# Performance work log

Measured on AMD Instinct MI355X. Metric: run time of the kernel, lower is better.

## Reference

```python
import jax, jax.numpy as jnp
import numpy as np

S, B, I, H, L, D = 512, 64, 128, 256, 6, 2  # seq, batch, input, hidden, layers, directions


def setup_inputs() -> dict:
    key = jax.random.key(0)
    ks = jax.random.split(key, 7)
    stdv = 1.0 / np.sqrt(H)
    u = lambda k, shape: jax.random.uniform(k, shape, jnp.float32, -stdv, stdv)
    return {
        "x": jax.random.normal(ks[0], (S, B, I), jnp.float32),
        "h0": jax.random.normal(ks[1], (L * D, B, H), jnp.float32),
        "w_ih0": u(ks[2], (D, 3 * H, I)),            # layer 0 input weights
        "w_ih": u(ks[3], (L - 1, D, 3 * H, D * H)),  # layers 1.. input weights
        "w_hh": u(ks[4], (L, D, 3 * H, H)),
        "b_ih": u(ks[5], (L, D, 3 * H)),
        "b_hh": u(ks[6], (L, D, 3 * H)),
    }


def _gru_direction(gate_x, w_hh, b_hh, h0, reverse):
    # gate_x: (S, B, 3H) precomputed x @ W_ih.T + b_ih; scan the recurrence.
    def step(h, gx):
        gh = h @ w_hh.T + b_hh  # (B, 3H)
        x_r, x_z, x_n = jnp.split(gx, 3, axis=-1)
        h_r, h_z, h_n = jnp.split(gh, 3, axis=-1)
        r = jax.nn.sigmoid(x_r + h_r)
        z = jax.nn.sigmoid(x_z + h_z)
        n = jnp.tanh(x_n + r * h_n)
        h_new = (1.0 - z) * n + z * h
        return h_new, h_new

    h_last, ys = jax.lax.scan(step, h0, gate_x, reverse=reverse)
    return h_last, ys  # ys aligned with input time order even when reverse=True


def reference(x, h0, w_ih0, w_ih, w_hh, b_ih, b_hh):
    num_layers = w_hh.shape[0]
    inp = x  # (S, B, in_dim)
    h_n = []
    for layer in range(num_layers):
        outs = []
        for d in range(2):
            w = w_ih0[d] if layer == 0 else w_ih[layer - 1, d]
            # Single GEMM over the whole sequence for the input gates.
            gate_x = jnp.einsum('sbi,gi->sbg', inp, w) + b_ih[layer, d]
            h_last, ys = _gru_direction(
                gate_x, w_hh[layer, d], b_hh[layer, d],
                h0[layer * 2 + d], reverse=(d == 1))
            outs.append(ys)
            h_n.append(h_last)
        inp = jnp.concatenate(outs, axis=-1)  # (S, B, 2H)
    return jnp.stack(h_n)  # (L*2, B, H)
```

## Files before the change

kernel.cpp:

```cpp
#include <hip/hip_runtime.h>
#include <stdint.h>

#define S_LEN 512
#define NB    64
#define HID   256
#define G3    768
#define SB    32768
#define NLAYER 6

typedef short bf16x8 __attribute__((ext_vector_type(8)));
typedef short bf16x4 __attribute__((ext_vector_type(4)));
typedef float floatx4 __attribute__((ext_vector_type(4)));
typedef unsigned short u16;
typedef unsigned int   u32;

__device__ __forceinline__ float bf2f(u16 v) {
  u32 u = ((u32)v) << 16;
  return __builtin_bit_cast(float, u);
}
__device__ __forceinline__ u16 f2bf(float f) {
  u32 u = __builtin_bit_cast(u32, f);
  u = (u + 0x7FFFu + ((u >> 16) & 1u)) >> 16;
  return (u16)u;
}
__device__ __forceinline__ float fsigmoid(float x) {
  return __builtin_amdgcn_rcpf(1.0f + __expf(-x));
}
__device__ __forceinline__ float ftanh(float x) {
  return 1.0f - 2.0f * __builtin_amdgcn_rcpf(1.0f + __expf(x + x));
}
__device__ __forceinline__ u32 pk_bf16(float lo, float hi) {
  u32 r;
  asm("v_cvt_pk_bf16_f32 %0, %1, %2" : "=v"(r) : "v"(lo), "v"(hi));
  return r;
}

__device__ __forceinline__ void lds_barrier() {
  asm volatile("s_waitcnt lgkmcnt(0)\n\ts_barrier" ::: "memory");
}

__global__ void detect_fp32(const u16* __restrict__ x, int n, int* flag) {
  __shared__ int tot;
  if (threadIdx.x == 0) tot = 0;
  __syncthreads();
  int c = 0;
  for (int i = threadIdx.x; i < n; i += blockDim.x) {
    u16 v = x[i];
    if (((v >> 7) & 0xFF) == 0xFF) ++c;
  }
  atomicAdd(&tot, c);
  __syncthreads();
  if (threadIdx.x == 0) *flag = (tot > 64) ? 1 : 0;
}

__global__ void cvt(const void* __restrict__ src, u16* __restrict__ dst,
                    int n, const int* __restrict__ flag) {
  const int stride = gridDim.x * blockDim.x;
  const bool isf32 = (*flag != 0);
  for (int i = blockIdx.x * blockDim.x + threadIdx.x; i < n; i += stride) {
    if (isf32) dst[i] = f2bf(((const float*)src)[i]);
    else       dst[i] = ((const u16*)src)[i];
  }
}

__global__ void prep_bias(const u16* __restrict__ bih, const u16* __restrict__ bhh,
                          float* __restrict__ bc, int n) {
  int i = blockIdx.x * blockDim.x + threadIdx.x;
  if (i >= n) return;
  int col = i % G3;
  float v = bf2f(bih[i]);
  if (col < 512) v += bf2f(bhh[i]);
  bc[i] = v;
}

__global__ void write_out(const float* __restrict__ hNs, void* __restrict__ out,
                          int n, const int* __restrict__ flag) {
  int i = blockIdx.x * blockDim.x + threadIdx.x;
  if (i >= n) return;
  if (*flag) ((float*)out)[i] = hNs[i];
  else       ((u16*)out)[i]   = f2bf(hNs[i]);
}

__global__ __launch_bounds__(256)
void gate_gemm(const u16* __restrict__ A, const u16* __restrict__ W,
               const float* __restrict__ bias, u16* __restrict__ outg, int K) {
  const int m0  = blockIdx.x * 128;
  const int n0  = blockIdx.y * 128;
  const int dir = blockIdx.z;
  W    += (size_t)dir * G3 * K;
  bias += (size_t)dir * G3;
  outg += (size_t)dir * (size_t)SB * G3;

  __shared__ __align__(16) u16 lA[8192];
  __shared__ __align__(16) u16 lB[8192];

  const int tid  = threadIdx.x;
  const int lane = tid & 63;
  const int wv   = tid >> 6;
  const int wm   = wv & 1, wn = wv >> 1;
  const int l15  = lane & 15, quad = lane >> 4;

  floatx4 acc[4][4] = {};

  for (int k0 = 0; k0 < K; k0 += 64) {
    bf16x8 ra[4], rb[4];
#pragma unroll
    for (int i = 0; i < 4; ++i) {
      int c   = i * 256 + tid;
      int row = c >> 3;
      int kc  = (c & 7) ^ (row & 7);
      ra[i] = *(const bf16x8*)(A + (size_t)(m0 + row) * K + (k0 + kc * 8));
      rb[i] = *(const bf16x8*)(W + (size_t)(n0 + row) * K + (k0 + kc * 8));
    }
    __syncthreads();
#pragma unroll
    for (int i = 0; i < 4; ++i) {
      *(bf16x8*)(lA + (size_t)(i * 256 + tid) * 8) = ra[i];
      *(bf16x8*)(lB + (size_t)(i * 256 + tid) * 8) = rb[i];
    }
    __syncthreads();

#pragma unroll
    for (int kt = 0; kt < 2; ++kt) {
      bf16x8 af[4], bfr[4];
#pragma unroll
      for (int mt = 0; mt < 4; ++mt) {
        int row = wm * 64 + mt * 16 + l15;
        int ch  = row * 8 + ((kt * 4 + quad) ^ (row & 7));
        af[mt] = *(const bf16x8*)(lA + ch * 8);
      }
#pragma unroll
      for (int nt = 0; nt < 4; ++nt) {
        int row = wn * 64 + nt * 16 + l15;
        int ch  = row * 8 + ((kt * 4 + quad) ^ (row & 7));
        bfr[nt] = *(const bf16x8*)(lB + ch * 8);
      }
#pragma unroll
      for (int mt = 0; mt < 4; ++mt)
#pragma unroll
        for (int nt = 0; nt < 4; ++nt)
          acc[mt][nt] = __builtin_amdgcn_mfma_f32_16x16x32_bf16(
              af[mt], bfr[nt], acc[mt][nt], 0, 0, 0);
    }
  }

  const int sIdx = (m0 >> 6) + wm;
#pragma unroll
  for (int nt = 0; nt < 4; ++nt) {
    int n    = n0 + wn * 64 + nt * 16 + l15;
    int g    = n >> 8, jc = n & 255;
    float bv = bias[n];
#pragma unroll
    for (int mt = 0; mt < 4; ++mt) {
      bf16x4 pk;
#pragma unroll
      for (int r = 0; r < 4; ++r) pk[r] = (short)f2bf(acc[mt][nt][r] + bv);
      *(bf16x4*)(outg + ((((size_t)mt * 512 + sIdx) * 256 + jc) * 3 + g) * 16 +
                 quad * 4) = pk;
    }
  }
}

__global__ __launch_bounds__(512)
__attribute__((amdgpu_waves_per_eu(2, 2)))
void gru_scan(const u16* __restrict__ gateX,
              const u16* __restrict__ Whh,
              const u16* __restrict__ Bhh,
              const u16* __restrict__ H0,
              u16* __restrict__ layerOut,
              float* __restrict__ hNs,
              int layer) {
  const int dir = blockIdx.x & 1;
  const int bg  = blockIdx.x >> 1;
  const int tid = threadIdx.x;
  const int lane = tid & 63;
  const int wv   = tid >> 6;
  const int l15  = lane & 15, quad = lane >> 4;

  __shared__ __align__(16) u16 wnL[65536];
  __shared__ __align__(16) u16 hb2[2][4096];

  const u16* Wd = Whh + (size_t)dir * G3 * HID;

#pragma unroll
  for (int i = 0; i < 16; ++i) {
    int ci = i * 512 + tid;
    int n  = ci >> 5;
    int c  = ci & 31;
    bf16x8 v = *(const bf16x8*)(Wd + (size_t)(512 + n) * HID + c * 8);
    *(bf16x8*)(wnL + c * 2048 + n * 8) = v;
  }

  bf16x8 wrz[8][2][2];
#pragma unroll
  for (int g = 0; g < 2; ++g)
#pragma unroll
    for (int nt = 0; nt < 2; ++nt) {
      int n = g * 256 + wv * 32 + nt * 16 + l15;
#pragma unroll
      for (int kt = 0; kt < 8; ++kt)
        wrz[kt][g][nt] = *(const bf16x8*)(Wd + (size_t)n * HID + kt * 32 + quad * 8);
    }
#pragma unroll
  for (int kt = 0; kt < 8; ++kt)
#pragma unroll
    for (int g = 0; g < 2; ++g)
#pragma unroll
      for (int nt = 0; nt < 2; ++nt)
        asm volatile("" : "+v"(wrz[kt][g][nt]));

  float bhn[2];
#pragma unroll
  for (int nt = 0; nt < 2; ++nt)
    bhn[nt] = bf2f(Bhh[dir * G3 + 512 + wv * 32 + nt * 16 + l15]);

  const int mrow = quad * 4;
  const int b0   = bg * 16 + mrow;

  const int afb    = quad * 128 + l15 * 8;
  const int bnb0   = quad * 2048 + (wv * 32 + l15) * 8;
  const int bnb1   = bnb0 + 16 * 8;
  int wb[2];
#pragma unroll
  for (int nt = 0; nt < 2; ++nt)
    wb[nt] = (wv * 4 + nt * 2 + (l15 >> 3)) * 128 + quad * 32 + (l15 & 7);

  {
    int row = tid >> 5, slot = tid & 31;
    const u16* hp = H0 + ((size_t)(layer * 2 + dir) * NB + bg * 16 + row) * HID + slot * 8;
    *(bf16x8*)(&hb2[0][slot * 128 + row * 8]) = *(const bf16x8*)hp;
  }
  float hreg[2][4];
#pragma unroll
  for (int nt = 0; nt < 2; ++nt)
#pragma unroll
    for (int r = 0; r < 4; ++r)
      hreg[nt][r] = bf2f(H0[((size_t)(layer * 2 + dir) * NB + b0 + r) * HID +
                            wv * 32 + nt * 16 + l15]);

  const long sstep = dir ? -(long)(256 * 3 * 16) : (long)(256 * 3 * 16);
  const u16* xb;
  {
    const int s0 = dir ? (S_LEN - 1) : 0;
    xb = gateX + (size_t)dir * SB * G3 +
         ((((size_t)bg * 512 + s0) * 256 + (wv * 32 + l15)) * 3) * 16 + quad * 4;
  }
  bf16x4 xp[3][2];
#pragma unroll
  for (int g = 0; g < 3; ++g)
#pragma unroll
    for (int nt = 0; nt < 2; ++nt)
      xp[g][nt] = *(const bf16x4*)(xb + nt * 768 + g * 16);
  xb += sstep;

  u16* loPtr;
  {
    int row = tid >> 5, slot = tid & 31;
    const int sFirst = dir ? (S_LEN - 1) : 0;
    loPtr = layerOut + ((size_t)sFirst * NB + bg * 16 + row) * 512 +
            dir * HID + slot * 8;
  }
  const long lostep = dir ? -(long)(NB * 512) : (long)(NB * 512);

  lds_barrier();

  for (int t = 0; t < S_LEN; ++t) {
    const int cur = t & 1, nxt = cur ^ 1;

    floatx4 aR[2], aZ[2], aN[2];
    bf16x4 xn0 = xp[2][0], xn1 = xp[2][1];
#pragma unroll
    for (int nt = 0; nt < 2; ++nt)
#pragma unroll
      for (int r = 0; r < 4; ++r) {
        aR[nt][r] = bf2f((u16)xp[0][nt][r]);
        aZ[nt][r] = bf2f((u16)xp[1][nt][r]);
        aN[nt][r] = bhn[nt];
      }

#pragma unroll
    for (int g = 0; g < 3; ++g)
#pragma unroll
      for (int nt = 0; nt < 2; ++nt)
        xp[g][nt] = *(const bf16x4*)(xb + nt * 768 + g * 16);
    if (t < S_LEN - 1) xb += sstep;

    if (t > 0) {
      int row = tid >> 5, slot = tid & 31;
      bf16x8 hv = *(const bf16x8*)(&hb2[cur][slot * 128 + row * 8]);
      *(bf16x8*)loPtr = hv;
      loPtr += lostep;
    }

#pragma unroll
    for (int kt = 0; kt < 8; ++kt) {
      bf16x8 af  = *(const bf16x8*)(&hb2[cur][afb + kt * 512]);
      bf16x8 bn0 = *(const bf16x8*)(wnL + bnb0 + kt * 8192);
      bf16x8 bn1 = *(const bf16x8*)(wnL + bnb1 + kt * 8192);
      aR[0] = __builtin_amdgcn_mfma_f32_16x16x32_bf16(af, wrz[kt][0][0], aR[0], 0, 0, 0);
      aR[1] = __builtin_amdgcn_mfma_f32_16x16x32_bf16(af, wrz[kt][0][1], aR[1], 0, 0, 0);
      aZ[0] = __builtin_amdgcn_mfma_f32_16x16x32_bf16(af, wrz[kt][1][0], aZ[0], 0, 0, 0);
      aZ[1] = __builtin_amdgcn_mfma_f32_16x16x32_bf16(af, wrz[kt][1][1], aZ[1], 0, 0, 0);
      aN[0] = __builtin_amdgcn_mfma_f32_16x16x32_bf16(af, bn0,           aN[0], 0, 0, 0);
      aN[1] = __builtin_amdgcn_mfma_f32_16x16x32_bf16(af, bn1,           aN[1], 0, 0, 0);
    }

#pragma unroll
    for (int nt = 0; nt < 2; ++nt) {
      const bf16x4 xn = nt ? xn1 : xn0;
#pragma unroll
      for (int r = 0; r < 4; ++r) {
        float rg = fsigmoid(aR[nt][r]);
        float zg = fsigmoid(aZ[nt][r]);
        float ng = ftanh(bf2f((u16)xn[r]) + rg * aN[nt][r]);
        float hn = ng + zg * (hreg[nt][r] - ng);
        hreg[nt][r] = hn;
        hb2[nxt][wb[nt] + r * 8] = f2bf(hn);
      }
    }

    lds_barrier();
  }

  {
    int row = tid >> 5, slot = tid & 31;
    const int sLast = dir ? 0 : (S_LEN - 1);
    bf16x8 hv = *(const bf16x8*)(&hb2[0][slot * 128 + row * 8]);
    *(bf16x8*)(layerOut + ((size_t)sLast * NB + bg * 16 + row) * 512 +
               dir * HID + slot * 8) = hv;
  }
#pragma unroll
  for (int nt = 0; nt < 2; ++nt)
#pragma unroll
    for (int r = 0; r < 4; ++r)
      hNs[((size_t)(layer * 2 + dir) * NB + b0 + r) * HID +
          wv * 32 + nt * 16 + l15] = hreg[nt][r];
}

extern "C" void kernel_launch(void* const* d_in, const int* in_sizes, int n_in,
                              void* d_out, int out_size, void* d_ws, size_t ws_size,
                              hipStream_t stream) {
  (void)n_in; (void)ws_size;
  char* ws = (char*)d_ws;
  int*   flag  = (int*)ws;
  float* hNs   = (float*)(ws + 4096);
  float* biasC = (float*)(ws + 790528);
  u16*   h0C   = (u16*)(ws + (1u << 20));
  u16*   wih0C = h0C   + 196608;
  u16*   wihC  = wih0C + 196608;
  u16*   whhC  = wihC  + 3932160;
  u16*   bihC  = whhC  + 2359296;
  u16*   bhhC  = bihC  + 9216;
  u16*   gateX = (u16*)(ws + (16u  << 20));
  u16*   bufA  = (u16*)(ws + (112u << 20));
  u16*   bufB  = (u16*)(ws + (144u << 20));
  u16*   xC    = bufB;

  detect_fp32<<<1, 1024, 0, stream>>>((const u16*)d_in[0], 262144, flag);
  cvt<<<512, 256, 0, stream>>>(d_in[0], xC,    in_sizes[0], flag);
  cvt<<<256, 256, 0, stream>>>(d_in[1], h0C,   in_sizes[1], flag);
  cvt<<<256, 256, 0, stream>>>(d_in[2], wih0C, in_sizes[2], flag);
  cvt<<<512, 256, 0, stream>>>(d_in[3], wihC,  in_sizes[3], flag);
  cvt<<<512, 256, 0, stream>>>(d_in[4], whhC,  in_sizes[4], flag);
  cvt<<< 64, 256, 0, stream>>>(d_in[5], bihC,  in_sizes[5], flag);
  cvt<<< 64, 256, 0, stream>>>(d_in[6], bhhC,  in_sizes[6], flag);
  prep_bias<<<36, 256, 0, stream>>>(bihC, bhhC, biasC, NLAYER * 2 * G3);

  for (int layer = 0; layer < NLAYER; ++layer) {
    const u16* inp = (layer == 0) ? xC : ((layer & 1) ? bufA : bufB);
    u16* outBuf    = (layer & 1) ? bufB : bufA;

    const int K = (layer == 0) ? 128 : 512;
    const u16* W = (layer == 0) ? wih0C
                                : (wihC + (size_t)(layer - 1) * 2 * G3 * 512);
    dim3 grid(256, 6, 2);
    gate_gemm<<<grid, 256, 0, stream>>>(inp, W, biasC + (size_t)layer * 2 * G3,
                                        gateX, K);
    gru_scan<<<8, 512, 0, stream>>>(gateX, whhC + (size_t)layer * 2 * G3 * HID,
                                    bhhC + (size_t)layer * 2 * G3, h0C,
                                    outBuf, hNs, layer);
  }
  write_out<<<(out_size + 255) / 256, 256, 0, stream>>>(hNs, d_out, out_size, flag);
}
```

Baseline: 5.964 ms.

## Keep most of W_hn in registers and drop fp32 hidden-state registers

The n-gate recurrent weights for the first six of eight K-tiles now live in VGPRs, and only the last two K-tiles stay in LDS. This shrinks the LDS footprint and cuts per-step LDS traffic in the MFMA loop. To free registers, the fp32 hidden state is no longer carried across steps; it is re-read from the bf16 LDS buffer each step, and the final h_n is written from bf16. The trade is higher register pressure and reduced precision of the carried state, since the blend now uses a bf16-rounded previous h.

```diff
diff --git a/kernel.cpp b/kernel.cpp
--- a/kernel.cpp
+++ b/kernel.cpp
@@ -28,11 +28,6 @@
 }
 __device__ __forceinline__ float ftanh(float x) {
   return 1.0f - 2.0f * __builtin_amdgcn_rcpf(1.0f + __expf(x + x));
-}
-__device__ __forceinline__ u32 pk_bf16(float lo, float hi) {
-  u32 r;
-  asm("v_cvt_pk_bf16_f32 %0, %1, %2" : "=v"(r) : "v"(lo), "v"(hi));
-  return r;
 }
 
 __device__ __forceinline__ void lds_barrier() {
@@ -177,21 +172,22 @@
   const int wv   = tid >> 6;
   const int l15  = lane & 15, quad = lane >> 4;
 
-  __shared__ __align__(16) u16 wnL[65536];
+  __shared__ __align__(16) u16 wnL[16384];
   __shared__ __align__(16) u16 hb2[2][4096];
 
   const u16* Wd = Whh + (size_t)dir * G3 * HID;
 
 #pragma unroll
-  for (int i = 0; i < 16; ++i) {
+  for (int i = 0; i < 4; ++i) {
     int ci = i * 512 + tid;
-    int n  = ci >> 5;
-    int c  = ci & 31;
-    bf16x8 v = *(const bf16x8*)(Wd + (size_t)(512 + n) * HID + c * 8);
-    *(bf16x8*)(wnL + c * 2048 + n * 8) = v;
+    int n  = ci >> 3;
+    int kc = ci & 7;
+    bf16x8 v = *(const bf16x8*)(Wd + (size_t)(512 + n) * HID + (24 + kc) * 8);
+    *(bf16x8*)(wnL + kc * 2048 + n * 8) = v;
   }
 
   bf16x8 wrz[8][2][2];
+  bf16x8 wn6[6][2];
 #pragma unroll
   for (int g = 0; g < 2; ++g)
 #pragma unroll
@@ -202,24 +198,32 @@
         wrz[kt][g][nt] = *(const bf16x8*)(Wd + (size_t)n * HID + kt * 32 + quad * 8);
     }
 #pragma unroll
+  for (int nt = 0; nt < 2; ++nt) {
+    int n = 512 + wv * 32 + nt * 16 + l15;
+#pragma unroll
+    for (int kt = 0; kt < 6; ++kt)
+      wn6[kt][nt] = *(const bf16x8*)(Wd + (size_t)n * HID + kt * 32 + quad * 8);
+  }
+#pragma unroll
   for (int kt = 0; kt < 8; ++kt)
 #pragma unroll
     for (int g = 0; g < 2; ++g)
 #pragma unroll
       for (int nt = 0; nt < 2; ++nt)
         asm volatile("" : "+v"(wrz[kt][g][nt]));
+#pragma unroll
+  for (int kt = 0; kt < 6; ++kt)
+#pragma unroll
+    for (int nt = 0; nt < 2; ++nt)
+      asm volatile("" : "+v"(wn6[kt][nt]));
 
   float bhn[2];
 #pragma unroll
   for (int nt = 0; nt < 2; ++nt)
     bhn[nt] = bf2f(Bhh[dir * G3 + 512 + wv * 32 + nt * 16 + l15]);
 
-  const int mrow = quad * 4;
-  const int b0   = bg * 16 + mrow;
-
-  const int afb    = quad * 128 + l15 * 8;
-  const int bnb0   = quad * 2048 + (wv * 32 + l15) * 8;
-  const int bnb1   = bnb0 + 16 * 8;
+  const int afb = quad * 128 + l15 * 8;
+  const int bnb = quad * 2048 + (wv * 32 + l15) * 8;
   int wb[2];
 #pragma unroll
   for (int nt = 0; nt < 2; ++nt)
@@ -230,13 +234,6 @@
     const u16* hp = H0 + ((size_t)(layer * 2 + dir) * NB + bg * 16 + row) * HID + slot * 8;
     *(bf16x8*)(&hb2[0][slot * 128 + row * 8]) = *(const bf16x8*)hp;
   }
-  float hreg[2][4];
-#pragma unroll
-  for (int nt = 0; nt < 2; ++nt)
-#pragma unroll
-    for (int r = 0; r < 4; ++r)
-      hreg[nt][r] = bf2f(H0[((size_t)(layer * 2 + dir) * NB + b0 + r) * HID +
-                            wv * 32 + nt * 16 + l15]);
 
   const long sstep = dir ? -(long)(256 * 3 * 16) : (long)(256 * 3 * 16);
   const u16* xb;
@@ -285,6 +282,13 @@
         xp[g][nt] = *(const bf16x4*)(xb + nt * 768 + g * 16);
     if (t < S_LEN - 1) xb += sstep;
 
+    u16 hp[2][4];
+#pragma unroll
+    for (int nt = 0; nt < 2; ++nt)
+#pragma unroll
+      for (int r = 0; r < 4; ++r)
+        hp[nt][r] = hb2[cur][wb[nt] + r * 8];
+
     if (t > 0) {
       int row = tid >> 5, slot = tid & 31;
       bf16x8 hv = *(const bf16x8*)(&hb2[cur][slot * 128 + row * 8]);
@@ -294,9 +298,15 @@
 
 #pragma unroll
     for (int kt = 0; kt < 8; ++kt) {
-      bf16x8 af  = *(const bf16x8*)(&hb2[cur][afb + kt * 512]);
-      bf16x8 bn0 = *(const bf16x8*)(wnL + bnb0 + kt * 8192);
-      bf16x8 bn1 = *(const bf16x8*)(wnL + bnb1 + kt * 8192);
+      bf16x8 af = *(const bf16x8*)(&hb2[cur][afb + kt * 512]);
+      bf16x8 bn0, bn1;
+      if (kt < 6) {
+        bn0 = wn6[kt][0];
+        bn1 = wn6[kt][1];
+      } else {
+        bn0 = *(const bf16x8*)(wnL + bnb + (kt - 6) * 8192);
+        bn1 = *(const bf16x8*)(wnL + bnb + (kt - 6) * 8192 + 128);
+      }
       aR[0] = __builtin_amdgcn_mfma_f32_16x16x32_bf16(af, wrz[kt][0][0], aR[0], 0, 0, 0);
       aR[1] = __builtin_amdgcn_mfma_f32_16x16x32_bf16(af, wrz[kt][0][1], aR[1], 0, 0, 0);
       aZ[0] = __builtin_amdgcn_mfma_f32_16x16x32_bf16(af, wrz[kt][1][0], aZ[0], 0, 0, 0);
@@ -313,8 +323,8 @@
         float rg = fsigmoid(aR[nt][r]);
         float zg = fsigmoid(aZ[nt][r]);
         float ng = ftanh(bf2f((u16)xn[r]) + rg * aN[nt][r]);
-        float hn = ng + zg * (hreg[nt][r] - ng);
-        hreg[nt][r] = hn;
+        float h0 = bf2f(hp[nt][r]);
+        float hn = ng + zg * (h0 - ng);
         hb2[nxt][wb[nt] + r * 8] = f2bf(hn);
       }
     }
@@ -328,13 +338,15 @@
     bf16x8 hv = *(const bf16x8*)(&hb2[0][slot * 128 + row * 8]);
     *(bf16x8*)(layerOut + ((size_t)sLast * NB + bg * 16 + row) * 512 +
                dir * HID + slot * 8) = hv;
-  }
-#pragma unroll
-  for (int nt = 0; nt < 2; ++nt)
-#pragma unroll
-    for (int r = 0; r < 4; ++r)
-      hNs[((size_t)(layer * 2 + dir) * NB + b0 + r) * HID +
-          wv * 32 + nt * 16 + l15] = hreg[nt][r];
+    float* dst = hNs + ((size_t)(layer * 2 + dir) * NB + bg * 16 + row) * HID + slot * 8;
+    floatx4 v0, v1;
+#pragma unroll
+    for (int i = 0; i < 4; ++i) v0[i] = bf2f((u16)hv[i]);
+#pragma unroll
+    for (int i = 0; i < 4; ++i) v1[i] = bf2f((u16)hv[4 + i]);
+    *(floatx4*)dst = v0;
+    *((floatx4*)dst + 1) = v1;
+  }
 }
 
 extern "C" void kernel_launch(void* const* d_in, const int* in_sizes, int n_in,
```

Measured after the change: 5.263 ms. 1.13x faster.
